# Optimization experiments

Measured on AMD Instinct MI355X. Metric: run time of the kernel, lower is better.

Reference implementation:

```python
import jax, jax.numpy as jnp
import numpy as np

DM = 512; NH = 8; EL = 3; FACTOR = 3; EPS = 1e-5

def layernorm(x, g, b):
    m = x.mean(-1, keepdims=True)
    v = x.var(-1, keepdims=True)
    return (x - m) / jnp.sqrt(v + EPS) * g + b

def pos_embed(L, d):
    pos = jnp.arange(L, dtype=jnp.float32)[:, None]
    div = jnp.exp(jnp.arange(0, d, 2, dtype=jnp.float32) * (-np.log(10000.0) / d))
    pe = jnp.zeros((L, d), jnp.float32)
    pe = pe.at[:, 0::2].set(jnp.sin(pos * div))
    pe = pe.at[:, 1::2].set(jnp.cos(pos * div))
    return pe

def circ_conv1d(x, w, b=None):
    # x: [B,L,Cin], w: [Cout,Cin,3]; torch Conv1d padding=1, padding_mode='circular'
    xp = jnp.concatenate([x[:, -1:], x, x[:, :1]], axis=1)
    y = jax.lax.conv_general_dilated(xp, w, (1,), 'VALID', dimension_numbers=('NWC', 'OIW', 'NWC'))
    return y if b is None else y + b

def prob_attention(q, k, v, rng):
    # q,k,v: [B,H,L,D] -- Informer ProbSparse attention (non-masked encoder case)
    B, H, L, D = q.shape
    LK = k.shape[2]
    U = min(int(FACTOR * np.ceil(np.log(LK))), LK)   # sampled keys per query
    u = min(int(FACTOR * np.ceil(np.log(L))), L)     # top queries kept
    idx = jax.random.randint(rng, (L, U), 0, LK)     # shared across B,H as in torch
    k_samp = k[:, :, idx]                            # [B,H,L,U,D]
    qk = jnp.einsum('bhld,bhlud->bhlu', q, k_samp)
    M = qk.max(-1) - qk.sum(-1) / LK                 # sparsity measure
    top = jax.lax.top_k(M, u)[1]                     # [B,H,u]
    q_red = jnp.take_along_axis(q, top[..., None], axis=2)
    scores = jnp.einsum('bhud,bhkd->bhuk', q_red, k) / jnp.sqrt(jnp.asarray(D, q.dtype))
    attn = jax.nn.softmax(scores, axis=-1)
    upd = jnp.einsum('bhuk,bhkd->bhud', attn, v)
    ctx = jnp.broadcast_to(v.mean(axis=2, keepdims=True), (B, H, L, D))
    bi = jnp.arange(B)[:, None, None]
    hi = jnp.arange(H)[None, :, None]
    return ctx.at[bi, hi, top].set(upd)

def encoder_layer(x, p, rng):
    Wq_, bq_, Wk_, bk_, Wv_, bv_, Wo_, bo_, w1, b1, w2, b2, g1, be1, g2, be2 = p
    B, L, _ = x.shape
    D = DM // NH
    q = (x @ Wq_.T + bq_).reshape(B, L, NH, D).transpose(0, 2, 1, 3)
    k = (x @ Wk_.T + bk_).reshape(B, L, NH, D).transpose(0, 2, 1, 3)
    v = (x @ Wv_.T + bv_).reshape(B, L, NH, D).transpose(0, 2, 1, 3)
    ctx = prob_attention(q, k, v, rng).transpose(0, 2, 1, 3).reshape(B, L, DM)
    x = x + (ctx @ Wo_.T + bo_)
    x = layernorm(x, g1, be1)
    y = jax.nn.gelu(x @ w1.T + b1, approximate=False)  # pointwise conv1 (k=1)
    y = y @ w2.T + b2                                   # pointwise conv2 (k=1)
    return layernorm(x + y, g2, be2)

def distil_layer(x, w, b, g, beta):
    y = circ_conv1d(x, w, b)                 # Conv1d k=3 circular
    mu = y.mean((0, 1))
    var = y.var((0, 1))                      # BatchNorm1d, training stats
    y = (y - mu) / jnp.sqrt(var + EPS) * g + beta
    y = jax.nn.elu(y)
    # MaxPool1d(kernel=3, stride=2, padding=1)
    return jax.lax.reduce_window(y, -jnp.inf, jax.lax.max, (1, 3, 1), (1, 2, 1), ((0, 0), (1, 1), (0, 0)))

def setup_inputs():
    key = jax.random.key(0)
    ks = jax.random.split(key, 12)
    B, S, CIN, COUT, DFF = 8, 2048, 7, 7, 2048
    r = lambda k, s: jax.random.normal(k, s, jnp.float32)
    return {
        'x_enc': r(ks[0], (B, S, CIN)),
        'tok_w': r(ks[1], (DM, CIN, 3)) * (2.0 / (CIN * 3)) ** 0.5,
        'Wq': r(ks[2], (EL, DM, DM)) * DM ** -0.5, 'bq': jnp.zeros((EL, DM)),
        'Wk': r(ks[3], (EL, DM, DM)) * DM ** -0.5, 'bk': jnp.zeros((EL, DM)),
        'Wv': r(ks[4], (EL, DM, DM)) * DM ** -0.5, 'bv': jnp.zeros((EL, DM)),
        'Wo': r(ks[5], (EL, DM, DM)) * DM ** -0.5, 'bo': jnp.zeros((EL, DM)),
        'conv1_w': r(ks[6], (EL, DFF, DM)) * DM ** -0.5, 'conv1_b': jnp.zeros((EL, DFF)),
        'conv2_w': r(ks[7], (EL, DM, DFF)) * DFF ** -0.5, 'conv2_b': jnp.zeros((EL, DM)),
        'ln1_g': jnp.ones((EL, DM)), 'ln1_b': jnp.zeros((EL, DM)),
        'ln2_g': jnp.ones((EL, DM)), 'ln2_b': jnp.zeros((EL, DM)),
        'dconv_w': r(ks[8], (EL - 1, DM, DM, 3)) * (DM * 3) ** -0.5, 'dconv_b': jnp.zeros((EL - 1, DM)),
        'bn_g': jnp.ones((EL - 1, DM)), 'bn_b': jnp.zeros((EL - 1, DM)),
        'lnf_g': jnp.ones((DM,)), 'lnf_b': jnp.zeros((DM,)),
        'end_w': r(ks[9], (COUT, DM)) * DM ** -0.5, 'end_b': jnp.zeros((COUT,)),
    }

def reference(x_enc, tok_w, Wq, bq, Wk, bk, Wv, bv, Wo, bo, conv1_w, conv1_b, conv2_w, conv2_b, ln1_g, ln1_b, ln2_g, ln2_b, dconv_w, dconv_b, bn_g, bn_b, lnf_g, lnf_b, end_w, end_b):
    x = circ_conv1d(x_enc, tok_w) + pos_embed(x_enc.shape[1], DM)  # DataEmbedding
    base = jax.random.key(42)
    for l in range(EL):
        p = (Wq[l], bq[l], Wk[l], bk[l], Wv[l], bv[l], Wo[l], bo[l],
             conv1_w[l], conv1_b[l], conv2_w[l], conv2_b[l],
             ln1_g[l], ln1_b[l], ln2_g[l], ln2_b[l])
        x = encoder_layer(x, p, jax.random.fold_in(base, l))
        if l < EL - 1:
            x = distil_layer(x, dconv_w[l], dconv_b[l], bn_g[l], bn_b[l])
    x = layernorm(x, lnf_g, lnf_b)
    return x @ end_w.T + end_b  # end_conv2 (Conv1d k=1)
```

## Files before the change

### kernel.cpp

```cpp
#include <hip/hip_runtime.h>
#include <cstdint>
#include <cstddef>

#define DMODEL 512
#define NHEAD 8
#define HD 64

typedef float f32x4 __attribute__((ext_vector_type(4)));
typedef _Float16 f16x8 __attribute__((ext_vector_type(8)));
typedef _Float16 f16x4 __attribute__((ext_vector_type(4)));

__device__ __forceinline__ uint32_t rotl32(uint32_t x, int r) {
  return (x << r) | (x >> (32 - r));
}

__device__ __forceinline__ void tf_block(uint32_t k0, uint32_t k1,
                                         uint32_t& x0, uint32_t& x1) {
  uint32_t ks0 = k0, ks1 = k1, ks2 = k0 ^ k1 ^ 0x1BD11BDAu;
  x0 += ks0; x1 += ks1;
  x0 += x1; x1 = rotl32(x1, 13); x1 ^= x0;
  x0 += x1; x1 = rotl32(x1, 15); x1 ^= x0;
  x0 += x1; x1 = rotl32(x1, 26); x1 ^= x0;
  x0 += x1; x1 = rotl32(x1, 6);  x1 ^= x0;
  x0 += ks1; x1 += ks2 + 1u;
  x0 += x1; x1 = rotl32(x1, 17); x1 ^= x0;
  x0 += x1; x1 = rotl32(x1, 29); x1 ^= x0;
  x0 += x1; x1 = rotl32(x1, 16); x1 ^= x0;
  x0 += x1; x1 = rotl32(x1, 24); x1 ^= x0;
  x0 += ks2; x1 += ks0 + 2u;
  x0 += x1; x1 = rotl32(x1, 13); x1 ^= x0;
  x0 += x1; x1 = rotl32(x1, 15); x1 ^= x0;
  x0 += x1; x1 = rotl32(x1, 26); x1 ^= x0;
  x0 += x1; x1 = rotl32(x1, 6);  x1 ^= x0;
  x0 += ks0; x1 += ks1 + 3u;
  x0 += x1; x1 = rotl32(x1, 17); x1 ^= x0;
  x0 += x1; x1 = rotl32(x1, 29); x1 ^= x0;
  x0 += x1; x1 = rotl32(x1, 16); x1 ^= x0;
  x0 += x1; x1 = rotl32(x1, 24); x1 ^= x0;
  x0 += ks1; x1 += ks2 + 4u;
  x0 += x1; x1 = rotl32(x1, 13); x1 ^= x0;
  x0 += x1; x1 = rotl32(x1, 15); x1 ^= x0;
  x0 += x1; x1 = rotl32(x1, 26); x1 ^= x0;
  x0 += x1; x1 = rotl32(x1, 6);  x1 ^= x0;
  x0 += ks2; x1 += ks0 + 5u;
}

__global__ void idx_kernel(int* __restrict__ idxb, int n, int layer, int mask) {
  int e = blockIdx.x * 256 + threadIdx.x;
  if (e >= n) return;
  uint32_t f0 = 0u, f1 = (uint32_t)layer;
  tf_block(0u, 42u, f0, f1);
  uint32_t s0 = 0u, s1 = 1u;
  tf_block(f0, f1, s0, s1);
  uint32_t x0 = 0u, x1 = (uint32_t)e;
  tf_block(s0, s1, x0, x1);
  uint32_t bits = x0 ^ x1;
  idxb[e] = (int)(bits & (uint32_t)mask);
}

__device__ __forceinline__ float gelu_f(float v) {
  return 0.5f * v * (1.0f + erff(v * 0.7071067811865476f));
}

template <int ACT, int HASR, int CONV, int PART, int PREC, int FUSE3>
__global__ __launch_bounds__(256, 2) void gemm128(
    const float* __restrict__ A, const void* __restrict__ Wsp,
    const float* __restrict__ bias, const float* Rres, float* C, float* C2,
    float* C3, int N, int K, int Lmask, int ntx, int nty, int kloop, int ks) {
  __shared__ __align__(16) _Float16 sm[4][128][32];
  const _Float16* Wh = (const _Float16*)Wsp;
  const _Float16* Wl = Wh + (size_t)N * K;
  const int tid = threadIdx.x;
  int blk = blockIdx.x;
  const int tiles = ntx * nty;
  int kb = 0;
  if (PART) { kb = blk / tiles; blk -= kb * tiles; }
  const int koff = kb * kloop;
  const int xcd = blk & 7;
  const int j = blk >> 3;
  const int jr = j / ntx;
  const int row_t = xcd * (nty >> 3) + jr;
  const int col_t = j - jr * ntx;
  const int row0 = row_t * 128, col0 = col_t * 128;

  const int r4 = tid >> 2;
  const int ss = tid & 3;

  const float* Ap0 = A + (size_t)(row0 + r4) * K + koff + ss * 8;
  const float* Ap1 = A + (size_t)(row0 + 64 + r4) * K + koff + ss * 8;
  const _Float16* Wh0 = Wh + (size_t)(col0 + r4) * K + koff + ss * 8;
  const _Float16* Wh1 = Wh + (size_t)(col0 + 64 + r4) * K + koff + ss * 8;
  const _Float16* Wl0 = Wl + (size_t)(col0 + r4) * K + koff + ss * 8;
  const _Float16* Wl1 = Wl + (size_t)(col0 + 64 + r4) * K + koff + ss * 8;
  int tcv0 = 0, bb0 = 0, tcv1 = 0, bb1 = 0;
  if (CONV) {
    int a0 = row0 + r4, a1 = row0 + 64 + r4;
    tcv0 = a0 & Lmask; bb0 = a0 & ~Lmask;
    tcv1 = a1 & Lmask; bb1 = a1 & ~Lmask;
  }

  const int lane = tid & 63;
  const int wv = tid >> 6;
  const int wr = (wv >> 1) << 6;
  const int wc = (wv & 1) << 6;
  const int fr = lane & 15;
  const int fs = lane >> 4;

  f32x4 acc[4][4];
  {
    f32x4 z = {0.f, 0.f, 0.f, 0.f};
#pragma unroll
    for (int r = 0; r < 4; ++r)
#pragma unroll
      for (int c = 0; c < 4; ++c) acc[r][c] = z;
  }

  f32x4 ra[4], rwh[2], rwl[2];

  auto gload = [&](int k0) {
    const float *a0p, *a1p;
    if (CONV) {
      int kabs = koff + k0 + ss * 8;
      int w = kabs >> 9, cq = kabs & 511;
      a0p = A + (size_t)(bb0 | ((tcv0 - 1 + w) & Lmask)) * 512 + cq;
      a1p = A + (size_t)(bb1 | ((tcv1 - 1 + w) & Lmask)) * 512 + cq;
    } else {
      a0p = Ap0 + k0;
      a1p = Ap1 + k0;
    }
    ra[0] = *(const f32x4*)(a0p);
    ra[1] = *(const f32x4*)(a0p + 4);
    ra[2] = *(const f32x4*)(a1p);
    ra[3] = *(const f32x4*)(a1p + 4);
    rwh[0] = *(const f32x4*)(Wh0 + k0);
    rwh[1] = *(const f32x4*)(Wh1 + k0);
    if (PREC == 3) {
      rwl[0] = *(const f32x4*)(Wl0 + k0);
      rwl[1] = *(const f32x4*)(Wl1 + k0);
    }
  };

  const int T = kloop >> 5;
  gload(0);

  for (int it = 0; it < T; ++it) {
#pragma unroll
    for (int p = 0; p < 2; ++p) {
      const int row = (p << 6) + r4;
      const int sl = (ss ^ ((row >> 1) & 3)) << 3;
      float tmp[8];
      *(f32x4*)(tmp) = ra[2 * p];
      *(f32x4*)(tmp + 4) = ra[2 * p + 1];
      _Float16 hv[8], lv[8];
#pragma unroll
      for (int q = 0; q < 8; ++q) {
        _Float16 h = (_Float16)tmp[q];
        hv[q] = h;
        if (PREC == 3) lv[q] = (_Float16)(tmp[q] - (float)h);
      }
      *(f16x8*)&sm[0][row][sl] = *(f16x8*)hv;
      if (PREC == 3) *(f16x8*)&sm[1][row][sl] = *(f16x8*)lv;
      *(f32x4*)&sm[2][row][sl] = rwh[p];
      if (PREC == 3) *(f32x4*)&sm[3][row][sl] = rwl[p];
    }
    __syncthreads();
    if (it + 1 < T) gload((it + 1) << 5);
    f16x8 wfh[4], wfl[4], afh[4], afl[4];
#pragma unroll
    for (int c = 0; c < 4; ++c) {
      const int row = wc + (c << 4) + fr;
      const int sl = (fs ^ ((row >> 1) & 3)) << 3;
      wfh[c] = *(const f16x8*)&sm[2][row][sl];
      if (PREC == 3) wfl[c] = *(const f16x8*)&sm[3][row][sl];
    }
#pragma unroll
    for (int r = 0; r < 4; ++r) {
      const int row = wr + (r << 4) + fr;
      const int sl = (fs ^ ((row >> 1) & 3)) << 3;
      afh[r] = *(const f16x8*)&sm[0][row][sl];
      if (PREC == 3) afl[r] = *(const f16x8*)&sm[1][row][sl];
    }
#pragma unroll
    for (int r = 0; r < 4; ++r)
#pragma unroll
      for (int c = 0; c < 4; ++c) {
        acc[r][c] = __builtin_amdgcn_mfma_f32_16x16x32_f16(afh[r], wfh[c],
                                                           acc[r][c], 0, 0, 0);
        if (PREC == 3) {
          acc[r][c] = __builtin_amdgcn_mfma_f32_16x16x32_f16(
              afh[r], wfl[c], acc[r][c], 0, 0, 0);
          acc[r][c] = __builtin_amdgcn_mfma_f32_16x16x32_f16(
              afl[r], wfh[c], acc[r][c], 0, 0, 0);
        }
      }
    __syncthreads();
  }

  const int crow = fs << 2;
  if (PART) {
    float* Cp = C + (size_t)kb * ((size_t)(nty << 7)) * N;
#pragma unroll
    for (int r = 0; r < 4; ++r) {
      const int m0 = row0 + wr + (r << 4) + crow;
#pragma unroll
      for (int c = 0; c < 4; ++c) {
        const int n0 = col0 + wc + (c << 4) + fr;
#pragma unroll
        for (int q = 0; q < 4; ++q)
          Cp[(size_t)(m0 + q) * N + n0] = acc[r][c][q];
      }
    }
  } else if (FUSE3) {
    const int grp = col0 >> 9;
    float* Cb = (grp == 0) ? C : ((grp == 1) ? C2 : C3);
#pragma unroll
    for (int r = 0; r < 4; ++r) {
      const int m0 = row0 + wr + (r << 4) + crow;
#pragma unroll
      for (int c = 0; c < 4; ++c) {
        const int n0 = col0 + wc + (c << 4) + fr;
        const int cl = n0 & 511;
        const float bcol = bias[n0];
#pragma unroll
        for (int q = 0; q < 4; ++q)
          Cb[(size_t)(m0 + q) * 512 + cl] = acc[r][c][q] + bcol;
      }
    }
  } else {
#pragma unroll
    for (int r = 0; r < 4; ++r) {
      const int m0 = row0 + wr + (r << 4) + crow;
#pragma unroll
      for (int c = 0; c < 4; ++c) {
        const int n0 = col0 + wc + (c << 4) + fr;
        const float bcol = bias[n0];
#pragma unroll
        for (int q = 0; q < 4; ++q) {
          float v = acc[r][c][q] + bcol;
          if (HASR) v += Rres[(size_t)(m0 + q) * N + n0];
          if (ACT == 1) v = gelu_f(v);
          C[(size_t)(m0 + q) * N + n0] = v;
        }
      }
    }
  }
}

template <int HASR>
__global__ __launch_bounds__(256) void combine_kernel(
    const float* __restrict__ part, const float* __restrict__ bias,
    const float* Rres, float* __restrict__ Cout, size_t MN, int ks) {
  size_t gid = (size_t)blockIdx.x * 256 + threadIdx.x;
  int c = (int)(gid & 511);
  float v = 0.f;
  for (int kb = 0; kb < ks; kb++) v += part[kb * MN + gid];
  v += bias[c];
  if (HASR) v += Rres[gid];
  Cout[gid] = v;
}

__global__ __launch_bounds__(256) void splitw_kernel(const float* __restrict__ w,
                                                     _Float16* __restrict__ o,
                                                     int n, int ps) {
  int g = (blockIdx.x * 256 + threadIdx.x) << 2;
  if (g >= n) return;
  f32x4 f = *(const f32x4*)(w + g);
  f16x4 hv, lv;
#pragma unroll
  for (int q = 0; q < 4; ++q) {
    _Float16 h = (_Float16)f[q];
    hv[q] = h;
    lv[q] = (_Float16)(f[q] - (float)h);
  }
  *(f16x4*)(o + g) = hv;
  *(f16x4*)(o + ps + g) = lv;
}

__global__ void biascat_kernel(const float* __restrict__ a,
                               const float* __restrict__ b,
                               const float* __restrict__ c,
                               float* __restrict__ o) {
  int g = blockIdx.x * 256 + threadIdx.x;
  if (g < 512) o[g] = a[g];
  else if (g < 1024) o[g] = b[g - 512];
  else if (g < 1536) o[g] = c[g - 1024];
}

__global__ void tokpe_kernel(const float* __restrict__ xe,
                             const float* __restrict__ w,
                             float* __restrict__ out, int S) {
  int gid = blockIdx.x * 256 + threadIdx.x;
  int o = gid & 511;
  int bt = gid >> 9;
  int t = bt % S, b = bt / S;
  float acc = 0.f;
#pragma unroll
  for (int ww = 0; ww < 3; ww++) {
    int tt = t - 1 + ww;
    tt = (tt < 0) ? tt + S : (tt >= S ? tt - S : tt);
    const float* xr = xe + ((size_t)(b * S + tt)) * 7;
#pragma unroll
    for (int i = 0; i < 7; i++) acc += xr[i] * w[o * 21 + i * 3 + ww];
  }
  int i2 = o >> 1;
  float dv = expf((float)(2 * i2) * (-9.210340371976184f / 512.0f));
  float ang = (float)t * dv;
  acc += (o & 1) ? cosf(ang) : sinf(ang);
  out[gid] = acc;
}

__global__ void packw_kernel(const float* __restrict__ dw,
                             _Float16* __restrict__ wp) {
  int gid = blockIdx.x * 256 + threadIdx.x;
  int o = gid / 1536;
  int kk = gid - o * 1536;
  int ww = kk / 512;
  int c = kk - ww * 512;
  float v = dw[((size_t)o * 512 + c) * 3 + ww];
  _Float16 h = (_Float16)v;
  wp[gid] = h;
  wp[786432 + gid] = (_Float16)(v - (float)h);
}

__global__ __launch_bounds__(256, 8) void mscore_kernel(
    const float* __restrict__ Q, const float* __restrict__ Kb,
    const int* __restrict__ idxb, float* __restrict__ Mout, int L, int U) {
  int i = blockIdx.x;
  int b = i & 7;
  int j = i >> 3;
  int tid = threadIdx.x;
  int qd = tid >> 2;
  int q = tid & 3;
  int h = qd & 7;
  int t = j * 8 + (qd >> 3);
  const float* qp = Q + ((size_t)(b * L + t)) * DMODEL + h * HD + q * 4;
  float4 qv0 = *(const float4*)(qp);
  float4 qv1 = *(const float4*)(qp + 16);
  float4 qv2 = *(const float4*)(qp + 32);
  float4 qv3 = *(const float4*)(qp + 48);
  const float* Kh = Kb + (size_t)b * L * DMODEL + h * HD + q * 4;
  const int* ip = idxb + t * U;
  float mx = -3.4e38f, sm = 0.f;
  int kr = ip[0];
  for (int jj = 0; jj < U; jj++) {
    const float* kp = Kh + (size_t)kr * DMODEL;
    float4 k0 = *(const float4*)(kp);
    float4 k1 = *(const float4*)(kp + 16);
    float4 k2 = *(const float4*)(kp + 32);
    float4 k3 = *(const float4*)(kp + 48);
    if (jj + 1 < U) kr = ip[jj + 1];
    float d = qv0.x * k0.x + qv0.y * k0.y + qv0.z * k0.z + qv0.w * k0.w +
              qv1.x * k1.x + qv1.y * k1.y + qv1.z * k1.z + qv1.w * k1.w +
              qv2.x * k2.x + qv2.y * k2.y + qv2.z * k2.z + qv2.w * k2.w +
              qv3.x * k3.x + qv3.y * k3.y + qv3.z * k3.z + qv3.w * k3.w;
    d += __shfl_xor(d, 1);
    d += __shfl_xor(d, 2);
    mx = fmaxf(mx, d);
    sm += d;
  }
  if (q == 0) Mout[(size_t)(b * 8 + h) * L + t] = mx - sm / (float)L;
}

__global__ __launch_bounds__(256) void topk_kernel(const float* __restrict__ Mv,
                                                   int* __restrict__ topb, int L,
                                                   int u) {
  __shared__ float wv_s[4];
  __shared__ int wi_s[4];
  __shared__ int best_s;
  int bh = blockIdx.x, tid = threadIdx.x;
  int lane = tid & 63, w = tid >> 6;
  int cnt = L >> 8;
  float lv[8];
  for (int i = 0; i < cnt; i++) lv[i] = Mv[(size_t)bh * L + i * 256 + tid];
  for (int r = 0; r < u; r++) {
    float bv = -3.4e38f;
    int bi = 0x7fffffff;
    for (int i = 0; i < cnt; i++) {
      if (lv[i] > bv) { bv = lv[i]; bi = i * 256 + tid; }
    }
    for (int s = 32; s > 0; s >>= 1) {
      float ov = __shfl_down(bv, s);
      int oi = __shfl_down(bi, s);
      if (ov > bv || (ov == bv && oi < bi)) { bv = ov; bi = oi; }
    }
    if (lane == 0) { wv_s[w] = bv; wi_s[w] = bi; }
    __syncthreads();
    if (tid == 0) {
      float fv = wv_s[0];
      int fi = wi_s[0];
      for (int q = 1; q < 4; q++) {
        if (wv_s[q] > fv || (wv_s[q] == fv && wi_s[q] < fi)) {
          fv = wv_s[q];
          fi = wi_s[q];
        }
      }
      best_s = fi;
      topb[bh * u + r] = fi;
    }
    __syncthreads();
    int win = best_s;
    if ((win & 255) == tid) lv[win >> 8] = -3.4e38f;
  }
}

__global__ void gatherq_kernel(const float* __restrict__ Q,
                               const int* __restrict__ topb,
                               float* __restrict__ qsel, int L, int u) {
  int i = blockIdx.x;
  int bh = i / u;
  int b = bh >> 3, h = bh & 7;
  int t = topb[i];
  qsel[i * HD + threadIdx.x] =
      Q[((size_t)(b * L + t)) * DMODEL + h * HD + threadIdx.x];
}

__global__ __launch_bounds__(256) void xmean_kernel(const float* __restrict__ x,
                                                    float* __restrict__ psumx,
                                                    int L) {
  int i = blockIdx.x;
  int b = i >> 3, g = i & 7;
  int rows = L >> 3;
  int tid = threadIdx.x;
  const float* base = x + ((size_t)b * L + (size_t)g * rows) * DMODEL;
  float s0 = 0.f, s1 = 0.f;
  for (int t = 0; t < rows; t++) {
    s0 += base[(size_t)t * DMODEL + tid];
    s1 += base[(size_t)t * DMODEL + tid + 256];
  }
  psumx[i * DMODEL + tid] = s0;
  psumx[i * DMODEL + tid + 256] = s1;
}

__global__ __launch_bounds__(256) void mvmake_kernel(
    const float* __restrict__ psumx, const float* __restrict__ Wv,
    const float* __restrict__ bv, const float* __restrict__ Wo,
    const float* __restrict__ bo, float* __restrict__ mvg,
    float* __restrict__ mvWog, int L) {
  __shared__ float xm[512];
  __shared__ float mvs[512];
  int b = blockIdx.x, tid = threadIdx.x;
  float inv = 1.0f / (float)L;
  for (int nn = 0; nn < 2; nn++) {
    int c = tid + nn * 256;
    float s = 0.f;
    for (int g = 0; g < 8; g++) s += psumx[(b * 8 + g) * DMODEL + c];
    xm[c] = s * inv;
  }
  __syncthreads();
  for (int nn = 0; nn < 2; nn++) {
    int n = tid + nn * 256;
    const float* wr = Wv + (size_t)n * 512;
    float s = bv[n];
    for (int k = 0; k < 512; k += 4) {
      float4 w4 = *(const float4*)(wr + k);
      s += xm[k] * w4.x + xm[k + 1] * w4.y + xm[k + 2] * w4.z + xm[k + 3] * w4.w;
    }
    mvs[n] = s;
    mvg[b * DMODEL + n] = s;
  }
  __syncthreads();
  for (int nn = 0; nn < 2; nn++) {
    int n = tid + nn * 256;
    const float* wr = Wo + (size_t)n * 512;
    float s = bo[n];
    for (int k = 0; k < 512; k += 4) {
      float4 w4 = *(const float4*)(wr + k);
      s += mvs[k] * w4.x + mvs[k + 1] * w4.y + mvs[k + 2] * w4.z +
           mvs[k + 3] * w4.w;
    }
    mvWog[b * DMODEL + n] = s;
  }
}

__global__ void x1bcast_kernel(const float* __restrict__ x,
                               const float* __restrict__ mvWog,
                               float* __restrict__ x1, int L) {
  int gid = blockIdx.x * 256 + threadIdx.x;
  int c = gid & 511;
  int r = gid >> 9;
  int b = r / L;
  x1[gid] = x[gid] + mvWog[b * DMODEL + c];
}

__global__ __launch_bounds__(256) void attnflash_kernel(
    const float* __restrict__ qsel, const float* __restrict__ Kb,
    const float* __restrict__ Vb, float* __restrict__ pm,
    float* __restrict__ pl, float* __restrict__ pO, int L, int u, int nchunk) {
  __shared__ float qs[24][64];
  __shared__ float Kt[64][68];
  __shared__ float Ps[24][68];
  int blk = blockIdx.x;
  int bh = blk / nchunk;
  int c = blk - bh * nchunk;
  int b = bh >> 3, h = bh & 7;
  int cs = L / nchunk;
  int tid = threadIdx.x;
  int lane = tid & 63;
  int w = tid >> 6;
  for (int i = tid; i < u * 64; i += 256)
    qs[i >> 6][i & 63] = qsel[(size_t)bh * u * 64 + i];
  float m[6], l[6], O[6];
#pragma unroll
  for (int k = 0; k < 6; k++) { m[k] = -3.4e38f; l[k] = 0.f; O[k] = 0.f; }
  const float* Kbase = Kb + (size_t)b * L * DMODEL + h * HD;
  const float* Vbase = Vb + (size_t)b * L * DMODEL + h * HD;
  const int jrow = tid & 63;
  const int dch = (tid >> 6) << 4;
  for (int j0 = c * cs; j0 < (c + 1) * cs; j0 += 64) {
    __syncthreads();
    const float* kr = Kbase + (size_t)(j0 + jrow) * DMODEL + dch;
    float4 k0 = *(const float4*)(kr);
    float4 k1 = *(const float4*)(kr + 4);
    float4 k2 = *(const float4*)(kr + 8);
    float4 k3 = *(const float4*)(kr + 12);
#pragma unroll
    for (int q = 0; q < 4; q++) {
      Kt[dch + q][jrow] = ((float*)&k0)[q];
      Kt[dch + 4 + q][jrow] = ((float*)&k1)[q];
      Kt[dch + 8 + q][jrow] = ((float*)&k2)[q];
      Kt[dch + 12 + q][jrow] = ((float*)&k3)[q];
    }
    __syncthreads();
#pragma unroll
    for (int k = 0; k < 6; k++) {
      int qi = 4 * k + w;
      if (qi >= u) break;
      float s = 0.f;
#pragma unroll
      for (int d = 0; d < 64; d++) s += qs[qi][d] * Kt[d][lane];
      s *= 0.125f;
      float mx = s;
#pragma unroll
      for (int off = 32; off > 0; off >>= 1)
        mx = fmaxf(mx, __shfl_down(mx, off));
      mx = __shfl(mx, 0);
      float mnew = fmaxf(m[k], mx);
      float p = expf(s - mnew);
      float ps = p;
#pragma unroll
      for (int off = 32; off > 0; off >>= 1) ps += __shfl_down(ps, off);
      ps = __shfl(ps, 0);
      float alpha = expf(m[k] - mnew);
      l[k] = l[k] * alpha + ps;
      m[k] = mnew;
      O[k] *= alpha;
      Ps[qi][lane] = p;
    }
    for (int j = 0; j < 64; j += 4) {
      float v0 = Vbase[(size_t)(j0 + j) * DMODEL + lane];
      float v1 = Vbase[(size_t)(j0 + j + 1) * DMODEL + lane];
      float v2 = Vbase[(size_t)(j0 + j + 2) * DMODEL + lane];
      float v3 = Vbase[(size_t)(j0 + j + 3) * DMODEL + lane];
#pragma unroll
      for (int k = 0; k < 6; k++) {
        int qi = 4 * k + w;
        if (qi >= u) break;
        O[k] += Ps[qi][j] * v0 + Ps[qi][j + 1] * v1 + Ps[qi][j + 2] * v2 +
                Ps[qi][j + 3] * v3;
      }
    }
  }
#pragma unroll
  for (int k = 0; k < 6; k++) {
    int qi = 4 * k + w;
    if (qi < u) {
      int p = (bh * nchunk + c) * u + qi;
      if (lane == 0) { pm[p] = m[k]; pl[p] = l[k]; }
      pO[(size_t)p * 64 + lane] = O[k];
    }
  }
}

__global__ __launch_bounds__(256) void deltaWo_kernel(
    const float* __restrict__ pm, const float* __restrict__ pl,
    const float* __restrict__ pO, const float* __restrict__ mvg,
    const int* __restrict__ topb, const float* __restrict__ Wo, float* x1,
    int L, int u, int nchunk) {
  __shared__ float ds[64];
  int sel = blockIdx.x;
  int bh = sel / u;
  int qi = sel - bh * u;
  int b = bh >> 3, h = bh & 7;
  int t = topb[sel];
  int tid = threadIdx.x;
  if (tid < 64) {
    float mstar = -3.4e38f;
    for (int c = 0; c < nchunk; c++)
      mstar = fmaxf(mstar, pm[(bh * nchunk + c) * u + qi]);
    float lstar = 0.f, O = 0.f;
    for (int c = 0; c < nchunk; c++) {
      int p = (bh * nchunk + c) * u + qi;
      float wgt = expf(pm[p] - mstar);
      lstar += wgt * pl[p];
      O += wgt * pO[(size_t)p * 64 + tid];
    }
    ds[tid] = O / lstar - mvg[b * DMODEL + h * HD + tid];
  }
  __syncthreads();
  float* row = x1 + ((size_t)(b * L + t)) * DMODEL;
  for (int nn = 0; nn < 2; nn++) {
    int n = tid + nn * 256;
    const float* wr = Wo + (size_t)n * 512 + h * HD;
    float a = 0.f;
#pragma unroll
    for (int k = 0; k < 64; k += 4) {
      float4 w4 = *(const float4*)(wr + k);
      a += ds[k] * w4.x + ds[k + 1] * w4.y + ds[k + 2] * w4.z + ds[k + 3] * w4.w;
    }
    atomicAdd(row + n, a);
  }
}

__global__ __launch_bounds__(256) void ln_kernel(const float* __restrict__ X,
                                                 const float* __restrict__ g,
                                                 const float* __restrict__ bta,
                                                 float* __restrict__ Y) {
  int row = blockIdx.x * 4 + (threadIdx.x >> 6);
  int lane = threadIdx.x & 63;
  size_t base = (size_t)row * DMODEL + lane * 8;
  float4 a = *(const float4*)(X + base);
  float4 b = *(const float4*)(X + base + 4);
  float s = a.x + a.y + a.z + a.w + b.x + b.y + b.z + b.w;
#pragma unroll
  for (int off = 32; off > 0; off >>= 1) s += __shfl_xor(s, off);
  float mean = s * (1.0f / 512.0f);
  float d[8];
  d[0] = a.x - mean; d[1] = a.y - mean; d[2] = a.z - mean; d[3] = a.w - mean;
  d[4] = b.x - mean; d[5] = b.y - mean; d[6] = b.z - mean; d[7] = b.w - mean;
  float q = 0.f;
#pragma unroll
  for (int i = 0; i < 8; ++i) q += d[i] * d[i];
#pragma unroll
  for (int off = 32; off > 0; off >>= 1) q += __shfl_xor(q, off);
  float inv = 1.0f / sqrtf(q * (1.0f / 512.0f) + 1e-5f);
  int col = lane * 8;
  float4 g0 = *(const float4*)(g + col);
  float4 g1 = *(const float4*)(g + col + 4);
  float4 t0 = *(const float4*)(bta + col);
  float4 t1 = *(const float4*)(bta + col + 4);
  float4 y0, y1;
  y0.x = d[0] * inv * g0.x + t0.x; y0.y = d[1] * inv * g0.y + t0.y;
  y0.z = d[2] * inv * g0.z + t0.z; y0.w = d[3] * inv * g0.w + t0.w;
  y1.x = d[4] * inv * g1.x + t1.x; y1.y = d[5] * inv * g1.y + t1.y;
  y1.z = d[6] * inv * g1.z + t1.z; y1.w = d[7] * inv * g1.w + t1.w;
  *(float4*)(Y + base) = y0;
  *(float4*)(Y + base + 4) = y1;
}

__global__ __launch_bounds__(256) void bnpart_kernel(const float* __restrict__ z,
                                                     float* __restrict__ psum,
                                                     float* __restrict__ psq,
                                                     int rowsPer) {
  int blk = blockIdx.x, tid = threadIdx.x;
  size_t r0 = (size_t)blk * rowsPer;
  float s0 = 0, q0 = 0, s1 = 0, q1 = 0;
  for (int r = 0; r < rowsPer; r++) {
    const float* zp = z + (r0 + r) * DMODEL;
    float a = zp[tid];
    s0 += a; q0 += a * a;
    float c = zp[tid + 256];
    s1 += c; q1 += c * c;
  }
  psum[blk * DMODEL + tid] = s0;
  psum[blk * DMODEL + tid + 256] = s1;
  psq[blk * DMODEL + tid] = q0;
  psq[blk * DMODEL + tid + 256] = q1;
}

__global__ void bnfin_kernel(const float* __restrict__ psum,
                             const float* __restrict__ psq, float* __restrict__ mu,
                             float* __restrict__ var, int nb, int Rtot) {
  int c = blockIdx.x * 256 + threadIdx.x;
  float s = 0, q = 0;
  for (int b = 0; b < nb; b++) {
    s += psum[b * DMODEL + c];
    q += psq[b * DMODEL + c];
  }
  float m = s / (float)Rtot;
  mu[c] = m;
  var[c] = fmaxf(q / (float)Rtot - m * m, 0.f);
}

__global__ void bnpool_kernel(const float* __restrict__ z,
                              const float* __restrict__ mu,
                              const float* __restrict__ var,
                              const float* __restrict__ g,
                              const float* __restrict__ bta,
                              float* __restrict__ out, int L) {
  int gid = blockIdx.x * 256 + threadIdx.x;
  int c = gid & 511;
  int bt = gid >> 9;
  int L2 = L >> 1;
  int t2 = bt % L2, b = bt / L2;
  float m = mu[c];
  float inv = 1.0f / sqrtf(var[c] + 1e-5f);
  float gg = g[c], bb = bta[c];
  float best = -3.4e38f;
#pragma unroll
  for (int ww = 0; ww < 3; ww++) {
    int t = 2 * t2 - 1 + ww;
    if (t < 0 || t >= L) continue;
    float yv = (z[((size_t)(b * L + t)) * DMODEL + c] - m) * inv * gg + bb;
    yv = (yv > 0.f) ? yv : expm1f(yv);
    best = fmaxf(best, yv);
  }
  out[gid] = best;
}

__global__ __launch_bounds__(64) void end_kernel(const float* __restrict__ xn,
                                                 const float* __restrict__ ew,
                                                 const float* __restrict__ eb,
                                                 float* __restrict__ out) {
  __shared__ float xs[512];
  __shared__ float red[64];
  int row = blockIdx.x, tid = threadIdx.x;
#pragma unroll
  for (int i = 0; i < 8; i++) xs[tid + 64 * i] = xn[(size_t)row * DMODEL + tid + 64 * i];
  __syncthreads();
  for (int c = 0; c < 7; c++) {
    float p = 0.f;
    for (int d = tid; d < 512; d += 64) p += xs[d] * ew[c * DMODEL + d];
    red[tid] = p;
    __syncthreads();
    for (int s = 32; s > 0; s >>= 1) {
      if (tid < s) red[tid] += red[tid + s];
      __syncthreads();
    }
    if (tid == 0) out[row * 7 + c] = red[0] + eb[c];
    __syncthreads();
  }
}

extern "C" void kernel_launch(void* const* d_in, const int* in_sizes, int n_in,
                              void* d_out, int out_size, void* d_ws,
                              size_t ws_size, hipStream_t stream) {
  (void)in_sizes; (void)n_in; (void)out_size;
  const float* x_enc = (const float*)d_in[0];
  const float* tok_w = (const float*)d_in[1];
  const float* Wq = (const float*)d_in[2];
  const float* bq = (const float*)d_in[3];
  const float* Wk = (const float*)d_in[4];
  const float* bk = (const float*)d_in[5];
  const float* Wv = (const float*)d_in[6];
  const float* bv = (const float*)d_in[7];
  const float* Wo = (const float*)d_in[8];
  const float* bo = (const float*)d_in[9];
  const float* w1 = (const float*)d_in[10];
  const float* b1 = (const float*)d_in[11];
  const float* w2 = (const float*)d_in[12];
  const float* b2 = (const float*)d_in[13];
  const float* g1 = (const float*)d_in[14];
  const float* be1 = (const float*)d_in[15];
  const float* g2 = (const float*)d_in[16];
  const float* be2 = (const float*)d_in[17];
  const float* dw = (const float*)d_in[18];
  const float* db = (const float*)d_in[19];
  const float* bng = (const float*)d_in[20];
  const float* bnb = (const float*)d_in[21];
  const float* lnfg = (const float*)d_in[22];
  const float* lnfb = (const float*)d_in[23];
  const float* endw = (const float*)d_in[24];
  const float* endb = (const float*)d_in[25];
  float* out = (float*)d_out;
  char* ws = (char*)d_ws;

  const int NCHMAX = 32;

  size_t o = 0;
  float* buf0 = (float*)(ws + o); o += (size_t)16384 * 512 * 4;
  float* qbuf = (float*)(ws + o); o += (size_t)16384 * 512 * 4;
  float* kbuf = (float*)(ws + o); o += (size_t)16384 * 512 * 4;
  float* wpack = (float*)(ws + o); o += (size_t)512 * 1536 * 4;
  float* Mb    = (float*)(ws + o); o += (size_t)64 * 2048 * 4;
  int*   idxb  = (int*)(ws + o);   o += (size_t)2048 * 24 * 4;
  int*   topb  = (int*)(ws + o);   o += 8192;
  float* qsel  = (float*)(ws + o); o += (size_t)64 * 24 * 64 * 4;
  float* mvg   = (float*)(ws + o); o += (size_t)8 * 512 * 4;
  float* mvWog = (float*)(ws + o); o += (size_t)8 * 512 * 4;
  float* psumx = (float*)(ws + o); o += (size_t)64 * 512 * 4;
  float* psum  = (float*)(ws + o); o += (size_t)128 * 512 * 4;
  float* psq   = (float*)(ws + o); o += (size_t)128 * 512 * 4;
  float* muv   = (float*)(ws + o); o += 2048;
  float* varv  = (float*)(ws + o); o += 2048;
  float* biasc = (float*)(ws + o); o += 8192;
  float* pmb   = (float*)(ws + o); o += (size_t)64 * NCHMAX * 24 * 4;
  float* plb   = (float*)(ws + o); o += (size_t)64 * NCHMAX * 24 * 4;
  float* pOb   = (float*)(ws + o); o += (size_t)64 * NCHMAX * 24 * 64 * 4;
  _Float16* w1s = (_Float16*)(ws + o); o += (size_t)2048 * 512 * 4;
  _Float16* w2s = (_Float16*)(ws + o); o += (size_t)512 * 2048 * 4;
  float* partb = (float*)(ws + o); o += (size_t)4 * 4096 * 2048;
  const bool uks = (ws_size >= o);
  float* vbuf = partb;
  float* chbuf = (float*)(ws + o); o += (size_t)16384 * 2048 * 4;
  const bool ubig = (ws_size >= o);

  const int B = 8;
  const int S = 2048;
  tokpe_kernel<<<B * S * DMODEL / 256, 256, 0, stream>>>(x_enc, tok_w, buf0, S);

  int L = S;
  const int Uarr[3] = {24, 21, 21};
  for (int l = 0; l < 3; l++) {
    int U = Uarr[l];
    int u = Uarr[l];
    int BL = B * L;
    int nty = BL >> 7;
    size_t MN = (size_t)BL * 512;
    int nch = L >> 6;
    idx_kernel<<<(L * U + 255) / 256, 256, 0, stream>>>(idxb, L * U, l, L - 1);

    splitw_kernel<<<256, 256, 0, stream>>>(Wq + (size_t)l * 262144, w1s,
                                           262144, 786432);
    splitw_kernel<<<256, 256, 0, stream>>>(Wk + (size_t)l * 262144,
                                           w1s + 262144, 262144, 786432);
    splitw_kernel<<<256, 256, 0, stream>>>(Wv + (size_t)l * 262144,
                                           w1s + 524288, 262144, 786432);
    biascat_kernel<<<6, 256, 0, stream>>>(bq + l * 512, bk + l * 512,
                                          bv + l * 512, biasc);
    gemm128<0, 0, 0, 0, 3, 1><<<nty * 12, 256, 0, stream>>>(
        buf0, w1s, biasc, nullptr, qbuf, kbuf, vbuf, 1536, 512, 0, 12, nty,
        512, 1);

    mscore_kernel<<<L, 256, 0, stream>>>(qbuf, kbuf, idxb, Mb, L, U);
    topk_kernel<<<64, 256, 0, stream>>>(Mb, topb, L, u);
    gatherq_kernel<<<64 * u, 64, 0, stream>>>(qbuf, topb, qsel, L, u);
    xmean_kernel<<<64, 256, 0, stream>>>(buf0, psumx, L);
    mvmake_kernel<<<8, 256, 0, stream>>>(psumx, Wv + (size_t)l * 262144,
                                         bv + l * 512, Wo + (size_t)l * 262144,
                                         bo + l * 512, mvg, mvWog, L);
    attnflash_kernel<<<64 * nch, 256, 0, stream>>>(qsel, kbuf, vbuf, pmb, plb,
                                                   pOb, L, u, nch);
    x1bcast_kernel<<<(unsigned)(MN / 256), 256, 0, stream>>>(buf0, mvWog, kbuf, L);
    deltaWo_kernel<<<64 * u, 256, 0, stream>>>(pmb, plb, pOb, mvg, topb,
                                               Wo + (size_t)l * 262144, kbuf, L,
                                               u, nch);
    ln_kernel<<<BL / 4, 256, 0, stream>>>(kbuf, g1 + l * 512, be1 + l * 512, qbuf);
    splitw_kernel<<<1024, 256, 0, stream>>>(w1 + (size_t)l * 1048576, w1s,
                                            1048576, 1048576);
    splitw_kernel<<<1024, 256, 0, stream>>>(w2 + (size_t)l * 1048576, w2s,
                                            1048576, 1048576);
    if (ubig) {
      gemm128<1, 0, 0, 0, 1, 0><<<16 * nty, 256, 0, stream>>>(
          qbuf, w1s, b1 + l * 2048, nullptr, chbuf, nullptr, nullptr, 2048,
          512, 0, 16, nty, 512, 1);
      if (4 * nty >= 256) {
        gemm128<0, 1, 0, 0, 1, 0><<<4 * nty, 256, 0, stream>>>(
            chbuf, w2s, b2 + l * 512, qbuf, kbuf, nullptr, nullptr, 512, 2048,
            0, 4, nty, 2048, 1);
      } else {
        gemm128<0, 0, 0, 1, 1, 0><<<4 * nty * 4, 256, 0, stream>>>(
            chbuf, w2s, nullptr, nullptr, partb, nullptr, nullptr, 512, 2048,
            0, 4, nty, 512, 4);
        combine_kernel<1><<<(unsigned)(MN / 256), 256, 0, stream>>>(
            partb, b2 + l * 512, qbuf, kbuf, MN, 4);
      }
    } else {
      for (int r0 = 0; r0 < BL; r0 += 4096) {
        gemm128<1, 0, 0, 0, 1, 0><<<16 * 32, 256, 0, stream>>>(
            qbuf + (size_t)r0 * 512, w1s, b1 + l * 2048, nullptr, buf0, nullptr,
            nullptr, 2048, 512, 0, 16, 32, 512, 1);
        if (uks) {
          gemm128<0, 0, 0, 1, 1, 0><<<4 * 32 * 4, 256, 0, stream>>>(
              buf0, w2s, nullptr, nullptr, partb, nullptr, nullptr, 512, 2048,
              0, 4, 32, 512, 4);
          combine_kernel<1><<<4096 * 512 / 256, 256, 0, stream>>>(
              partb, b2 + l * 512, qbuf + (size_t)r0 * 512,
              kbuf + (size_t)r0 * 512, (size_t)4096 * 512, 4);
        } else {
          gemm128<0, 1, 0, 0, 1, 0><<<4 * 32, 256, 0, stream>>>(
              buf0, w2s, b2 + l * 512, qbuf + (size_t)r0 * 512,
              kbuf + (size_t)r0 * 512, nullptr, nullptr, 512, 2048, 0, 4, 32,
              2048, 1);
        }
      }
    }
    ln_kernel<<<BL / 4, 256, 0, stream>>>(kbuf, g2 + l * 512, be2 + l * 512, buf0);

    if (l < 2) {
      packw_kernel<<<512 * 1536 / 256, 256, 0, stream>>>(
          dw + (size_t)l * 512 * 512 * 3, (_Float16*)wpack);
      int gqc = 4 * nty;
      int ksc = (gqc >= 512 || !uks) ? 1 : 2;
      if (ksc == 1) {
        gemm128<0, 0, 1, 0, 1, 0><<<gqc, 256, 0, stream>>>(
            buf0, wpack, db + l * 512, nullptr, kbuf, nullptr, nullptr, 512,
            1536, L - 1, 4, nty, 1536, 1);
      } else {
        gemm128<0, 0, 1, 1, 1, 0><<<gqc * 2, 256, 0, stream>>>(
            buf0, wpack, nullptr, nullptr, partb, nullptr, nullptr, 512, 1536,
            L - 1, 4, nty, 768, 2);
        combine_kernel<0><<<(unsigned)(MN / 256), 256, 0, stream>>>(
            partb, db + l * 512, nullptr, kbuf, MN, 2);
      }
      int nb = BL / 128;
      bnpart_kernel<<<nb, 256, 0, stream>>>(kbuf, psum, psq, 128);
      bnfin_kernel<<<2, 256, 0, stream>>>(psum, psq, muv, varv, nb, BL);
      bnpool_kernel<<<(BL / 2) * 512 / 256, 256, 0, stream>>>(
          kbuf, muv, varv, bng + l * 512, bnb + l * 512, buf0, L);
      L >>= 1;
    }
  }
  int BL = B * L;
  ln_kernel<<<BL / 4, 256, 0, stream>>>(buf0, lnfg, lnfb, qbuf);
  end_kernel<<<BL, 64, 0, stream>>>(qbuf, endw, endb, out);
}
```

Before: 1.668 ms.

## Store FFN hidden activations in fp16 and skip V low-part MFMAs

The first FFN GEMM now writes its GELU output as fp16, and the second FFN GEMM reads that fp16 buffer directly instead of loading fp32 and converting. This halves the traffic for the large hidden activation buffer and removes per-element conversions. Separately, the fused QKV GEMM skips the split-precision low-part loads and extra MFMAs for column tiles at or above 1024, which hold V. Both changes trade accuracy (fp16 intermediate, single-precision-split V projection) for less memory traffic and less compute.

```diff
diff --git a/kernel.cpp b/kernel.cpp
--- a/kernel.cpp
+++ b/kernel.cpp
@@ -62,14 +62,17 @@
   return 0.5f * v * (1.0f + erff(v * 0.7071067811865476f));
 }
 
-template <int ACT, int HASR, int CONV, int PART, int PREC, int FUSE3>
+template <int ACT, int HASR, int CONV, int PART, int PREC, int FUSE3, int AF16,
+          int OF16>
 __global__ __launch_bounds__(256, 2) void gemm128(
-    const float* __restrict__ A, const void* __restrict__ Wsp,
+    const void* __restrict__ A, const void* __restrict__ Wsp,
     const float* __restrict__ bias, const float* Rres, float* C, float* C2,
     float* C3, int N, int K, int Lmask, int ntx, int nty, int kloop, int ks) {
   __shared__ __align__(16) _Float16 sm[4][128][32];
   const _Float16* Wh = (const _Float16*)Wsp;
   const _Float16* Wl = Wh + (size_t)N * K;
+  const float* Afp = (const float*)A;
+  const _Float16* Af16 = (const _Float16*)A;
   const int tid = threadIdx.x;
   int blk = blockIdx.x;
   const int tiles = ntx * nty;
@@ -83,11 +86,13 @@
   const int col_t = j - jr * ntx;
   const int row0 = row_t * 128, col0 = col_t * 128;
 
+  const bool lo = (PREC == 3) && !(FUSE3 && col0 >= 1024);
+
   const int r4 = tid >> 2;
   const int ss = tid & 3;
 
-  const float* Ap0 = A + (size_t)(row0 + r4) * K + koff + ss * 8;
-  const float* Ap1 = A + (size_t)(row0 + 64 + r4) * K + koff + ss * 8;
+  const size_t aoff0 = (size_t)(row0 + r4) * K + koff + ss * 8;
+  const size_t aoff1 = (size_t)(row0 + 64 + r4) * K + koff + ss * 8;
   const _Float16* Wh0 = Wh + (size_t)(col0 + r4) * K + koff + ss * 8;
   const _Float16* Wh1 = Wh + (size_t)(col0 + 64 + r4) * K + koff + ss * 8;
   const _Float16* Wl0 = Wl + (size_t)(col0 + r4) * K + koff + ss * 8;
@@ -116,27 +121,36 @@
   }
 
   f32x4 ra[4], rwh[2], rwl[2];
+  f16x8 rah[2];
 
   auto gload = [&](int k0) {
-    const float *a0p, *a1p;
-    if (CONV) {
+    if (AF16) {
+      rah[0] = *(const f16x8*)(Af16 + aoff0 + k0);
+      rah[1] = *(const f16x8*)(Af16 + aoff1 + k0);
+    } else if (CONV) {
       int kabs = koff + k0 + ss * 8;
       int w = kabs >> 9, cq = kabs & 511;
-      a0p = A + (size_t)(bb0 | ((tcv0 - 1 + w) & Lmask)) * 512 + cq;
-      a1p = A + (size_t)(bb1 | ((tcv1 - 1 + w) & Lmask)) * 512 + cq;
+      const float* a0p =
+          Afp + (size_t)(bb0 | ((tcv0 - 1 + w) & Lmask)) * 512 + cq;
+      const float* a1p =
+          Afp + (size_t)(bb1 | ((tcv1 - 1 + w) & Lmask)) * 512 + cq;
+      ra[0] = *(const f32x4*)(a0p);
+      ra[1] = *(const f32x4*)(a0p + 4);
+      ra[2] = *(const f32x4*)(a1p);
+      ra[3] = *(const f32x4*)(a1p + 4);
     } else {
-      a0p = Ap0 + k0;
-      a1p = Ap1 + k0;
-    }
-    ra[0] = *(const f32x4*)(a0p);
-    ra[1] = *(const f32x4*)(a0p + 4);
-    ra[2] = *(const f32x4*)(a1p);
-    ra[3] = *(const f32x4*)(a1p + 4);
+      ra[0] = *(const f32x4*)(Afp + aoff0 + k0);
+      ra[1] = *(const f32x4*)(Afp + aoff0 + k0 + 4);
+      ra[2] = *(const f32x4*)(Afp + aoff1 + k0);
+      ra[3] = *(const f32x4*)(Afp + aoff1 + k0 + 4);
+    }
     rwh[0] = *(const f32x4*)(Wh0 + k0);
     rwh[1] = *(const f32x4*)(Wh1 + k0);
     if (PREC == 3) {
-      rwl[0] = *(const f32x4*)(Wl0 + k0);
-      rwl[1] = *(const f32x4*)(Wl1 + k0);
+      if (lo) {
+        rwl[0] = *(const f32x4*)(Wl0 + k0);
+        rwl[1] = *(const f32x4*)(Wl1 + k0);
+      }
     }
   };
 
@@ -148,20 +162,28 @@
     for (int p = 0; p < 2; ++p) {
       const int row = (p << 6) + r4;
       const int sl = (ss ^ ((row >> 1) & 3)) << 3;
-      float tmp[8];
-      *(f32x4*)(tmp) = ra[2 * p];
-      *(f32x4*)(tmp + 4) = ra[2 * p + 1];
-      _Float16 hv[8], lv[8];
-#pragma unroll
-      for (int q = 0; q < 8; ++q) {
-        _Float16 h = (_Float16)tmp[q];
-        hv[q] = h;
-        if (PREC == 3) lv[q] = (_Float16)(tmp[q] - (float)h);
-      }
-      *(f16x8*)&sm[0][row][sl] = *(f16x8*)hv;
-      if (PREC == 3) *(f16x8*)&sm[1][row][sl] = *(f16x8*)lv;
+      if (AF16) {
+        *(f16x8*)&sm[0][row][sl] = rah[p];
+      } else {
+        float tmp[8];
+        *(f32x4*)(tmp) = ra[2 * p];
+        *(f32x4*)(tmp + 4) = ra[2 * p + 1];
+        _Float16 hv[8], lv[8];
+#pragma unroll
+        for (int q = 0; q < 8; ++q) {
+          _Float16 h = (_Float16)tmp[q];
+          hv[q] = h;
+          if (PREC == 3) lv[q] = (_Float16)(tmp[q] - (float)h);
+        }
+        *(f16x8*)&sm[0][row][sl] = *(f16x8*)hv;
+        if (PREC == 3) {
+          if (lo) *(f16x8*)&sm[1][row][sl] = *(f16x8*)lv;
+        }
+      }
       *(f32x4*)&sm[2][row][sl] = rwh[p];
-      if (PREC == 3) *(f32x4*)&sm[3][row][sl] = rwl[p];
+      if (PREC == 3) {
+        if (lo) *(f32x4*)&sm[3][row][sl] = rwl[p];
+      }
     }
     __syncthreads();
     if (it + 1 < T) gload((it + 1) << 5);
@@ -171,28 +193,38 @@
       const int row = wc + (c << 4) + fr;
       const int sl = (fs ^ ((row >> 1) & 3)) << 3;
       wfh[c] = *(const f16x8*)&sm[2][row][sl];
-      if (PREC == 3) wfl[c] = *(const f16x8*)&sm[3][row][sl];
+      if (PREC == 3) {
+        if (lo) wfl[c] = *(const f16x8*)&sm[3][row][sl];
+      }
     }
 #pragma unroll
     for (int r = 0; r < 4; ++r) {
       const int row = wr + (r << 4) + fr;
       const int sl = (fs ^ ((row >> 1) & 3)) << 3;
       afh[r] = *(const f16x8*)&sm[0][row][sl];
-      if (PREC == 3) afl[r] = *(const f16x8*)&sm[1][row][sl];
+      if (PREC == 3) {
+        if (lo) afl[r] = *(const f16x8*)&sm[1][row][sl];
+      }
     }
 #pragma unroll
     for (int r = 0; r < 4; ++r)
 #pragma unroll
-      for (int c = 0; c < 4; ++c) {
+      for (int c = 0; c < 4; ++c)
         acc[r][c] = __builtin_amdgcn_mfma_f32_16x16x32_f16(afh[r], wfh[c],
                                                            acc[r][c], 0, 0, 0);
-        if (PREC == 3) {
-          acc[r][c] = __builtin_amdgcn_mfma_f32_16x16x32_f16(
-              afh[r], wfl[c], acc[r][c], 0, 0, 0);
-          acc[r][c] = __builtin_amdgcn_mfma_f32_16x16x32_f16(
-              afl[r], wfh[c], acc[r][c], 0, 0, 0);
-        }
-      }
+    if (PREC == 3) {
+      if (lo) {
+#pragma unroll
+        for (int r = 0; r < 4; ++r)
+#pragma unroll
+          for (int c = 0; c < 4; ++c) {
+            acc[r][c] = __builtin_amdgcn_mfma_f32_16x16x32_f16(
+                afh[r], wfl[c], acc[r][c], 0, 0, 0);
+            acc[r][c] = __builtin_amdgcn_mfma_f32_16x16x32_f16(
+                afl[r], wfh[c], acc[r][c], 0, 0, 0);
+          }
+      }
+    }
     __syncthreads();
   }
 
@@ -239,7 +271,11 @@
           float v = acc[r][c][q] + bcol;
           if (HASR) v += Rres[(size_t)(m0 + q) * N + n0];
           if (ACT == 1) v = gelu_f(v);
-          C[(size_t)(m0 + q) * N + n0] = v;
+          if (OF16) {
+            ((_Float16*)C)[(size_t)(m0 + q) * N + n0] = (_Float16)v;
+          } else {
+            C[(size_t)(m0 + q) * N + n0] = v;
+          }
         }
       }
     }
@@ -793,6 +829,7 @@
   float* vbuf = partb;
   float* chbuf = (float*)(ws + o); o += (size_t)16384 * 2048 * 4;
   const bool ubig = (ws_size >= o);
+  _Float16* chbuf16 = (_Float16*)chbuf;
 
   const int B = 8;
   const int S = 2048;
@@ -817,7 +854,7 @@
                                            w1s + 524288, 262144, 786432);
     biascat_kernel<<<6, 256, 0, stream>>>(bq + l * 512, bk + l * 512,
                                           bv + l * 512, biasc);
-    gemm128<0, 0, 0, 0, 3, 1><<<nty * 12, 256, 0, stream>>>(
+    gemm128<0, 0, 0, 0, 3, 1, 0, 0><<<nty * 12, 256, 0, stream>>>(
         buf0, w1s, biasc, nullptr, qbuf, kbuf, vbuf, 1536, 512, 0, 12, nty,
         512, 1);
 
@@ -840,34 +877,34 @@
     splitw_kernel<<<1024, 256, 0, stream>>>(w2 + (size_t)l * 1048576, w2s,
                                             1048576, 1048576);
     if (ubig) {
-      gemm128<1, 0, 0, 0, 1, 0><<<16 * nty, 256, 0, stream>>>(
+      gemm128<1, 0, 0, 0, 1, 0, 0, 1><<<16 * nty, 256, 0, stream>>>(
           qbuf, w1s, b1 + l * 2048, nullptr, chbuf, nullptr, nullptr, 2048,
           512, 0, 16, nty, 512, 1);
       if (4 * nty >= 256) {
-        gemm128<0, 1, 0, 0, 1, 0><<<4 * nty, 256, 0, stream>>>(
-            chbuf, w2s, b2 + l * 512, qbuf, kbuf, nullptr, nullptr, 512, 2048,
-            0, 4, nty, 2048, 1);
+        gemm128<0, 1, 0, 0, 1, 0, 1, 0><<<4 * nty, 256, 0, stream>>>(
+            chbuf16, w2s, b2 + l * 512, qbuf, kbuf, nullptr, nullptr, 512,
+            2048, 0, 4, nty, 2048, 1);
       } else {
-        gemm128<0, 0, 0, 1, 1, 0><<<4 * nty * 4, 256, 0, stream>>>(
-            chbuf, w2s, nullptr, nullptr, partb, nullptr, nullptr, 512, 2048,
+        gemm128<0, 0, 0, 1, 1, 0, 1, 0><<<4 * nty * 4, 256, 0, stream>>>(
+            chbuf16, w2s, nullptr, nullptr, partb, nullptr, nullptr, 512, 2048,
             0, 4, nty, 512, 4);
         combine_kernel<1><<<(unsigned)(MN / 256), 256, 0, stream>>>(
             partb, b2 + l * 512, qbuf, kbuf, MN, 4);
       }
     } else {
       for (int r0 = 0; r0 < BL; r0 += 4096) {
-        gemm128<1, 0, 0, 0, 1, 0><<<16 * 32, 256, 0, stream>>>(
+        gemm128<1, 0, 0, 0, 1, 0, 0, 0><<<16 * 32, 256, 0, stream>>>(
             qbuf + (size_t)r0 * 512, w1s, b1 + l * 2048, nullptr, buf0, nullptr,
             nullptr, 2048, 512, 0, 16, 32, 512, 1);
         if (uks) {
-          gemm128<0, 0, 0, 1, 1, 0><<<4 * 32 * 4, 256, 0, stream>>>(
+          gemm128<0, 0, 0, 1, 1, 0, 0, 0><<<4 * 32 * 4, 256, 0, stream>>>(
               buf0, w2s, nullptr, nullptr, partb, nullptr, nullptr, 512, 2048,
               0, 4, 32, 512, 4);
           combine_kernel<1><<<4096 * 512 / 256, 256, 0, stream>>>(
               partb, b2 + l * 512, qbuf + (size_t)r0 * 512,
               kbuf + (size_t)r0 * 512, (size_t)4096 * 512, 4);
         } else {
-          gemm128<0, 1, 0, 0, 1, 0><<<4 * 32, 256, 0, stream>>>(
+          gemm128<0, 1, 0, 0, 1, 0, 0, 0><<<4 * 32, 256, 0, stream>>>(
               buf0, w2s, b2 + l * 512, qbuf + (size_t)r0 * 512,
               kbuf + (size_t)r0 * 512, nullptr, nullptr, 512, 2048, 0, 4, 32,
               2048, 1);
@@ -882,11 +919,11 @@
       int gqc = 4 * nty;
       int ksc = (gqc >= 512 || !uks) ? 1 : 2;
       if (ksc == 1) {
-        gemm128<0, 0, 1, 0, 1, 0><<<gqc, 256, 0, stream>>>(
+        gemm128<0, 0, 1, 0, 1, 0, 0, 0><<<gqc, 256, 0, stream>>>(
             buf0, wpack, db + l * 512, nullptr, kbuf, nullptr, nullptr, 512,
             1536, L - 1, 4, nty, 1536, 1);
       } else {
-        gemm128<0, 0, 1, 1, 1, 0><<<gqc * 2, 256, 0, stream>>>(
+        gemm128<0, 0, 1, 1, 1, 0, 0, 0><<<gqc * 2, 256, 0, stream>>>(
             buf0, wpack, nullptr, nullptr, partb, nullptr, nullptr, 512, 1536,
             L - 1, 4, nty, 768, 2);
         combine_kernel<0><<<(unsigned)(MN / 256), 256, 0, stream>>>(
```

Result: slower. 1.713 ms (+2.7%).
